# Performance work log

Hardware: AMD Instinct MI355X
Metric: run time of the kernel (lower is better)

## Reference

```python
import jax, jax.numpy as jnp
import numpy as np

B, N, D = 8, 10000, 16
E = 320000
EH, EOUT, NOUT = 32, 30, 64

def setup_inputs() -> dict:
    key = jax.random.key(0)
    ks = jax.random.split(key, 12)
    x = jax.random.normal(ks[0], (B, N, D), dtype=jnp.float32)
    edge_index = jax.random.randint(ks[1], (2, E), 0, N, dtype=jnp.int32)
    # edge_attr: col 0 = city distance (keep away from 0), col 1 = direction
    dist = jax.random.uniform(ks[2], (E,), dtype=jnp.float32) * 100.0 + 1.0
    direc = jax.random.uniform(ks[3], (E,), dtype=jnp.float32) * 360.0
    edge_attr = jnp.stack([dist, direc], axis=-1)
    wind_mean = jnp.array([3.0, 180.0], dtype=jnp.float32)
    wind_std = jnp.array([1.5, 90.0], dtype=jnp.float32)
    W1 = jax.random.normal(ks[4], (2 * D + 2 + 1, EH), dtype=jnp.float32) * 0.1
    b1 = jnp.zeros((EH,), dtype=jnp.float32)
    W2 = jax.random.normal(ks[5], (EH, EOUT), dtype=jnp.float32) * 0.1
    b2 = jnp.zeros((EOUT,), dtype=jnp.float32)
    Wn = jax.random.normal(ks[6], (EOUT, NOUT), dtype=jnp.float32) * 0.1
    bn = jnp.zeros((NOUT,), dtype=jnp.float32)
    return {"x": x, "edge_index": edge_index, "edge_attr": edge_attr,
            "wind_mean": wind_mean, "wind_std": wind_std,
            "W1": W1, "b1": b1, "W2": W2, "b2": b2, "Wn": Wn, "bn": bn}

def reference(x, edge_index, edge_attr, wind_mean, wind_std, W1, b1, W2, b2, Wn, bn):
    src, tgt = edge_index[0], edge_index[1]
    node_src = x[:, src]      # [B, E, D]
    node_tgt = x[:, tgt]      # [B, E, D]
    # de-normalize wind features (last 2 channels)
    src_wind = node_src[:, :, -2:] * wind_std[None, None, :] + wind_mean[None, None, :]
    speed = src_wind[:, :, 0]
    direc = src_wind[:, :, 1]
    city_dist = edge_attr[:, 0][None, :]   # [1, E]
    city_direc = edge_attr[:, 1][None, :]
    theta = jnp.abs(city_direc - direc)
    edge_weight = jax.nn.relu(3.0 * speed * jnp.cos(theta) / city_dist)  # [B, E]
    # normalized edge attributes (torch std is unbiased)
    ea_norm = (edge_attr - edge_attr.mean(axis=0)) / jnp.std(edge_attr, axis=0, ddof=1)
    ea_norm_b = jnp.broadcast_to(ea_norm[None, :, :], (x.shape[0], ea_norm.shape[0], 2))
    feat = jnp.concatenate([node_src, node_tgt, ea_norm_b, edge_weight[:, :, None]], axis=-1)  # [B, E, 2D+3]
    h = jax.nn.sigmoid(feat @ W1 + b1)
    e = jax.nn.sigmoid(h @ W2 + b2)        # [B, E, EOUT]
    agg = jnp.zeros((x.shape[0], x.shape[1], e.shape[-1]), dtype=e.dtype)
    agg = agg.at[:, tgt].add(e)
    agg = agg.at[:, src].add(-e)
    out = jax.nn.sigmoid(agg @ Wn + bn)    # [B, N, NOUT]
    return out
```

## Files before the change

kernel.cpp:

```cpp
#include <hip/hip_runtime.h>
#include <hip/hip_bf16.h>
#include <math.h>

#define B 8
#define N 10000
#define D 16
#define E 320000
#define EH 32
#define EOUT 30
#define NOUT 64
#define FEAT 35
#define FILL_BLOCKS ((E + 255) / 256)
#define PQ1K_BLOCKS ((B * N) / 16)

typedef short bf16x8 __attribute__((ext_vector_type(8)));
typedef float f32x4 __attribute__((ext_vector_type(4)));

#define LDS_FENCE() asm volatile("" ::: "memory")

__device__ __forceinline__ float sigmoidf_(float v) {
    return __builtin_amdgcn_rcpf(1.0f + __expf(-v));
}

__device__ __forceinline__ unsigned int pack_bf16_2(float a, float b) {
    unsigned ua = __float_as_uint(a), ub = __float_as_uint(b);
    ua = (ua + 0x7FFFu + ((ua >> 16) & 1u)) >> 16;
    ub = (ub + 0x7FFFu + ((ub >> 16) & 1u)) >> 16;
    return ua | (ub << 16);
}

__device__ __forceinline__ unsigned short bf16rn(float f) {
    unsigned u = __float_as_uint(f);
    u = (u + 0x7FFFu + ((u >> 16) & 1u)) >> 16;
    return (unsigned short)u;
}

__global__ void __launch_bounds__(256) stats_count_kernel(
    const float* __restrict__ ea, const int* __restrict__ eidx,
    float* __restrict__ stats, int* __restrict__ cnt)
{
    float s0 = 0.f, s1 = 0.f, q0 = 0.f, q1 = 0.f;
    for (int i = blockIdx.x * blockDim.x + threadIdx.x; i < E; i += gridDim.x * blockDim.x) {
        float2 v = *(const float2*)(ea + 2 * (size_t)i);
        s0 += v.x; q0 += v.x * v.x;
        s1 += v.y; q1 += v.y * v.y;
        atomicAdd(&cnt[eidx[E + i]], 1);
        atomicAdd(&cnt[N + eidx[i]], 1);
    }
    #pragma unroll
    for (int off = 32; off > 0; off >>= 1) {
        s0 += __shfl_down(s0, off);
        s1 += __shfl_down(s1, off);
        q0 += __shfl_down(q0, off);
        q1 += __shfl_down(q1, off);
    }
    if ((threadIdx.x & 63) == 0) {
        atomicAdd(&stats[0], s0);
        atomicAdd(&stats[1], s1);
        atomicAdd(&stats[2], q0);
        atomicAdd(&stats[3], q1);
    }
}

__global__ void __launch_bounds__(1024) scan_pq_kernel(
    const int* __restrict__ cnt_in, int* __restrict__ offs,
    int* __restrict__ cursor, float* __restrict__ stats,
    const float* __restrict__ W2, unsigned short* __restrict__ w2f,
    const float* __restrict__ x, const float* __restrict__ W1,
    const float* __restrict__ b1,
    unsigned short* __restrict__ Pb, unsigned short* __restrict__ Qb)
{
    if (blockIdx.x > 0) {
        int wid = (blockIdx.x - 1) * 16 + (threadIdx.x >> 6);
        int lane = threadIdx.x & 63;
        if (wid >= B * N) return;
        int j = lane & 31;
        int half = lane >> 5;
        const float* xr = x + (size_t)wid * D;
        float acc = half ? b1[j] : 0.f;
        const float* Wb = W1 + (half ? D * EH : 0);
        #pragma unroll
        for (int d = 0; d < D; d++)
            acc = fmaf(xr[d], Wb[d * EH + j], acc);
        float accN = __shfl_down(acc, 1);
        if (!(lane & 1)) {
            unsigned u = pack_bf16_2(acc, accN);
            unsigned short* dst = (half ? Qb : Pb) + (size_t)wid * EH + j;
            *(unsigned*)dst = u;
        }
        return;
    }

    if (threadIdx.x == 0) {
        const float n = (float)E;
        float s0 = stats[0], s1 = stats[1], q0 = stats[2], q1 = stats[3];
        float v0 = (q0 - s0 * s0 / n) / (n - 1.0f);
        float v1 = (q1 - s1 * s1 / n) / (n - 1.0f);
        stats[4] = s0 / n;
        stats[5] = 1.0f / sqrtf(v0);
        stats[6] = s1 / n;
        stats[7] = 1.0f / sqrtf(v1);
    }
    if (threadIdx.x < 128) {
        int tl = threadIdx.x >> 6;
        int ln = threadIdx.x & 63;
        int k0 = (ln >> 4) * 8;
        int col = tl * 16 + (ln & 15);
        unsigned short* hi = w2f + ((size_t)(tl * 2 + 0) * 64 + ln) * 8;
        unsigned short* lo = w2f + ((size_t)(tl * 2 + 1) * 64 + ln) * 8;
        #pragma unroll
        for (int j = 0; j < 8; j++) {
            float w = (col < EOUT) ? W2[(k0 + j) * EOUT + col] : 0.0f;
            unsigned u = __float_as_uint(w) & 0xFFFF0000u;
            float r = w - __uint_as_float(u);
            hi[j] = (unsigned short)(u >> 16);
            lo[j] = bf16rn(r);
        }
    }
    const int M = 2 * N;
    const int CH = 20;
    __shared__ int lds[1024];
    int t = threadIdx.x;
    int base = t * CH;
    int loc[CH];
    int s = 0;
    #pragma unroll
    for (int i = 0; i < CH; i++) {
        int idx = base + i;
        int v = (idx < M) ? cnt_in[idx] : 0;
        loc[i] = s;
        s += v;
    }
    lds[t] = s;
    __syncthreads();
    for (int off = 1; off < 1024; off <<= 1) {
        int v = (t >= off) ? lds[t - off] : 0;
        __syncthreads();
        lds[t] += v;
        __syncthreads();
    }
    int tbase = (t > 0) ? lds[t - 1] : 0;
    #pragma unroll
    for (int i = 0; i < CH; i++) {
        int idx = base + i;
        if (idx < M) {
            offs[idx] = tbase + loc[i];
            cursor[idx] = tbase + loc[i];
        }
    }
    if (t == 1023) offs[M] = lds[1023];
}

__global__ void __launch_bounds__(256) edge_mlp_kernel(
    const float* __restrict__ x, const int* __restrict__ eidx,
    const float* __restrict__ ea,
    const float* __restrict__ wind_mean, const float* __restrict__ wind_std,
    const float* __restrict__ W1, const float* __restrict__ b2,
    const float* __restrict__ stats,
    const unsigned short* __restrict__ Pb, const unsigned short* __restrict__ Qb,
    const unsigned short* __restrict__ w2f,
    unsigned short* __restrict__ eBuf,
    int* __restrict__ cursor, int* __restrict__ lists,
    int b0, int period, int ebOff)
{
    __shared__ unsigned short hsh[4][64][64];

    int bid = blockIdx.x;
    if (period) {
        int k = bid / period;
        int r = bid - k * period;
        if (r == period - 1) {
            int e = k * 256 + threadIdx.x;
            if (e < E) {
                int p = atomicAdd(&cursor[eidx[E + e]], 1);
                lists[p] = e;
                int q = atomicAdd(&cursor[N + eidx[e]], 1);
                lists[q] = e;
            }
            return;
        }
        bid -= k;
    }

    int t = bid * 256 + threadIdx.x;
    int bb = t / E;
    int e = t - bb * E;
    int b = b0 + bb;
    int wv = threadIdx.x >> 6;
    int lane = threadIdx.x & 63;

    int src = eidx[e];
    int tgt = eidx[E + e];

    const uint4* Pr = (const uint4*)(Pb + ((size_t)b * N + src) * EH);
    const uint4* Qr = (const uint4*)(Qb + ((size_t)b * N + tgt) * EH);

    float h[EH];
    #pragma unroll
    for (int i = 0; i < 4; i++) {
        uint4 p = Pr[i];
        uint4 q = Qr[i];
        unsigned pu[4] = {p.x, p.y, p.z, p.w};
        unsigned qu[4] = {q.x, q.y, q.z, q.w};
        #pragma unroll
        for (int k2 = 0; k2 < 4; k2++) {
            float pl = __uint_as_float(pu[k2] << 16);
            float ph = __uint_as_float(pu[k2] & 0xFFFF0000u);
            float ql = __uint_as_float(qu[k2] << 16);
            float qh = __uint_as_float(qu[k2] & 0xFFFF0000u);
            h[8 * i + 2 * k2 + 0] = pl + ql;
            h[8 * i + 2 * k2 + 1] = ph + qh;
        }
    }

    float2 eav = *(const float2*)(ea + 2 * (size_t)e);
    float dist = eav.x, cdir = eav.y;
    float f32v = (dist - stats[4]) * stats[5];
    float f33v = (cdir - stats[6]) * stats[7];

    float2 xw = *(const float2*)(x + ((size_t)b * N + src) * D + 14);
    float speed = xw.x * wind_std[0] + wind_mean[0];
    float sdir  = xw.y * wind_std[1] + wind_mean[1];
    float ew = fmaxf(3.0f * speed * __cosf(fabsf(cdir - sdir)) *
                     __builtin_amdgcn_rcpf(dist), 0.0f);

    const float* W1r32 = W1 + 32 * EH;
    const float* W1r33 = W1 + 33 * EH;
    const float* W1r34 = W1 + 34 * EH;
    #pragma unroll
    for (int j = 0; j < EH; j++) {
        float v = h[j];
        v = fmaf(f32v, W1r32[j], v);
        v = fmaf(f33v, W1r33[j], v);
        v = fmaf(ew,   W1r34[j], v);
        h[j] = sigmoidf_(v);
    }

    unsigned short* myrow = &hsh[wv][lane][0];
    int lx = lane & 7;
    #pragma unroll
    for (int i = 0; i < 4; i++) {
        unsigned hw[4];
        #pragma unroll
        for (int p = 0; p < 4; p++)
            hw[p] = pack_bf16_2(h[8 * i + 2 * p], h[8 * i + 2 * p + 1]);
        *(uint4*)(myrow + ((i ^ lx) << 3)) = make_uint4(hw[0], hw[1], hw[2], hw[3]);
    }
    LDS_FENCE();

    union { uint4 u; bf16x8 v; } bf[4];
    const uint4* wfp = (const uint4*)w2f;
    #pragma unroll
    for (int i = 0; i < 4; i++) bf[i].u = wfp[i * 64 + lane];

    int m  = lane & 15;
    int hr = lane >> 4;
    float bias0 = b2[m];
    float bias1 = (m < EOUT - 16) ? b2[16 + m] : 0.0f;

    f32x4 acc[4][2];
    #pragma unroll
    for (int g = 0; g < 4; g++) {
        f32x4 z0 = {bias0, bias0, bias0, bias0};
        f32x4 z1 = {bias1, bias1, bias1, bias1};
        acc[g][0] = z0;
        acc[g][1] = z1;
    }

    int mx = m & 7;
    #pragma unroll
    for (int g = 0; g < 4; g++) {
        const unsigned short* rp = &hsh[wv][g * 16 + m][0];
        bf16x8 Ah = *(const bf16x8*)(rp + ((hr ^ mx) << 3));
        acc[g][0] = __builtin_amdgcn_mfma_f32_16x16x32_bf16(Ah, bf[0].v, acc[g][0], 0, 0, 0);
        acc[g][1] = __builtin_amdgcn_mfma_f32_16x16x32_bf16(Ah, bf[2].v, acc[g][1], 0, 0, 0);
        acc[g][0] = __builtin_amdgcn_mfma_f32_16x16x32_bf16(Ah, bf[1].v, acc[g][0], 0, 0, 0);
        acc[g][1] = __builtin_amdgcn_mfma_f32_16x16x32_bf16(Ah, bf[3].v, acc[g][1], 0, 0, 0);
    }
    LDS_FENCE();

    unsigned short* wb = &hsh[wv][0][0];
    int c0 = m >> 3;
    int c1 = 2 + (m >> 3);
    int mp = m & 7;
    #pragma unroll
    for (int g = 0; g < 4; g++) {
        #pragma unroll
        for (int j = 0; j < 4; j++) {
            int er  = g * 16 + hr * 4 + j;
            int swz = ((hr & 1) << 2) | j;
            float v0 = sigmoidf_(acc[g][0][j]);
            float v1 = sigmoidf_(acc[g][1][j]);
            wb[er * 64 + ((c0 ^ swz) << 3) + mp] = bf16rn(v0);
            wb[er * 64 + ((c1 ^ swz) << 3) + mp] =
                (m < 14) ? bf16rn(v1) : (unsigned short)0;
        }
    }
    LDS_FENCE();

    int eWaveBase = e - lane;
    int rrow = lane >> 2;
    int rx   = rrow & 7;
    unsigned short* wdst = eBuf + ((size_t)(b - ebOff) * E + eWaveBase) * EH;
    #pragma unroll
    for (int i = 0; i < 4; i++) {
        uint4 v = *(const uint4*)(wb + (i * 16 + rrow) * 64 + (((lane & 3) ^ rx) << 3));
        *(uint4*)(wdst + i * 512 + lane * 8) = v;
    }
}

__global__ void __launch_bounds__(256) gather_kernel(
    const unsigned short* __restrict__ eBuf, const int* __restrict__ offs,
    const int* __restrict__ lists, const float* __restrict__ Wn,
    const float* __restrict__ bn, float* __restrict__ out,
    int b0, int nb, int ebOff)
{
    int wid = (blockIdx.x * blockDim.x + threadIdx.x) >> 6;
    int lane = threadIdx.x & 63;
    if (wid >= nb * N) return;
    int bb = wid / N;
    int node = wid - bb * N;
    int b = b0 + bb;

    int g = lane >> 2;
    int c = lane & 3;
    const uint4* ebase = (const uint4*)(eBuf + (size_t)(b - ebOff) * E * EH);

    float a0 = 0.f, a1 = 0.f, a2 = 0.f, a3 = 0.f;
    float a4 = 0.f, a5 = 0.f, a6 = 0.f, a7 = 0.f;

    {
        int s = offs[node], e1 = offs[node + 1];
        for (int r = s; r < e1; r += 16) {
            int row = r + g;
            if (row < e1) {
                int eid = lists[row];
                uint4 v = ebase[(size_t)eid * 4 + c];
                a0 += __uint_as_float(v.x << 16);
                a1 += __uint_as_float(v.x & 0xFFFF0000u);
                a2 += __uint_as_float(v.y << 16);
                a3 += __uint_as_float(v.y & 0xFFFF0000u);
                a4 += __uint_as_float(v.z << 16);
                a5 += __uint_as_float(v.z & 0xFFFF0000u);
                a6 += __uint_as_float(v.w << 16);
                a7 += __uint_as_float(v.w & 0xFFFF0000u);
            }
        }
    }
    {
        int s = offs[N + node], e1 = offs[N + node + 1];
        for (int r = s; r < e1; r += 16) {
            int row = r + g;
            if (row < e1) {
                int eid = lists[row];
                uint4 v = ebase[(size_t)eid * 4 + c];
                a0 -= __uint_as_float(v.x << 16);
                a1 -= __uint_as_float(v.x & 0xFFFF0000u);
                a2 -= __uint_as_float(v.y << 16);
                a3 -= __uint_as_float(v.y & 0xFFFF0000u);
                a4 -= __uint_as_float(v.z << 16);
                a5 -= __uint_as_float(v.z & 0xFFFF0000u);
                a6 -= __uint_as_float(v.w << 16);
                a7 -= __uint_as_float(v.w & 0xFFFF0000u);
            }
        }
    }

    #pragma unroll
    for (int off = 4; off <= 32; off <<= 1) {
        a0 += __shfl_xor(a0, off); a1 += __shfl_xor(a1, off);
        a2 += __shfl_xor(a2, off); a3 += __shfl_xor(a3, off);
        a4 += __shfl_xor(a4, off); a5 += __shfl_xor(a5, off);
        a6 += __shfl_xor(a6, off); a7 += __shfl_xor(a7, off);
    }

    float o = bn[lane];
    #pragma unroll
    for (int k = 0; k < EOUT; k++) {
        float av;
        switch (k & 7) {
            case 0:  av = a0; break;
            case 1:  av = a1; break;
            case 2:  av = a2; break;
            case 3:  av = a3; break;
            case 4:  av = a4; break;
            case 5:  av = a5; break;
            case 6:  av = a6; break;
            default: av = a7; break;
        }
        float ak = __shfl(av, k >> 3);
        o = fmaf(ak, Wn[k * NOUT + lane], o);
    }
    out[((size_t)b * N + node) * NOUT + lane] = sigmoidf_(o);
}

__global__ void __launch_bounds__(256) edge_kernel_atomic(
    const float* __restrict__ x, const int* __restrict__ eidx,
    const float* __restrict__ ea,
    const float* __restrict__ wind_mean, const float* __restrict__ wind_std,
    const float* __restrict__ W1, const float* __restrict__ b1,
    const float* __restrict__ W2, const float* __restrict__ b2,
    const float* __restrict__ stats, float* __restrict__ agg)
{
    int t = blockIdx.x * blockDim.x + threadIdx.x;
    if (t >= B * E) return;
    int b = t / E;
    int e = t - b * E;
    int src = eidx[e];
    int tgt = eidx[E + e];
    const float* xs = x + ((size_t)b * N + src) * D;
    const float* xt = x + ((size_t)b * N + tgt) * D;
    float f[FEAT];
    #pragma unroll
    for (int i = 0; i < D; i++) f[i] = xs[i];
    #pragma unroll
    for (int i = 0; i < D; i++) f[D + i] = xt[i];
    float2 eav = *(const float2*)(ea + 2 * (size_t)e);
    f[32] = (eav.x - stats[4]) * stats[5];
    f[33] = (eav.y - stats[6]) * stats[7];
    float speed = f[14] * wind_std[0] + wind_mean[0];
    float sdir  = f[15] * wind_std[1] + wind_mean[1];
    f[34] = fmaxf(3.0f * speed * cosf(fabsf(eav.y - sdir)) / eav.x, 0.0f);
    float h[EH];
    #pragma unroll
    for (int j = 0; j < EH; j++) h[j] = b1[j];
    #pragma unroll
    for (int k = 0; k < FEAT; k++) {
        float fk = f[k];
        #pragma unroll
        for (int j = 0; j < EH; j++) h[j] = fmaf(fk, W1[k * EH + j], h[j]);
    }
    #pragma unroll
    for (int j = 0; j < EH; j++) h[j] = sigmoidf_(h[j]);
    float o[EOUT];
    #pragma unroll
    for (int j = 0; j < EOUT; j++) o[j] = b2[j];
    #pragma unroll
    for (int k = 0; k < EH; k++) {
        float hk = h[k];
        #pragma unroll
        for (int j = 0; j < EOUT; j++) o[j] = fmaf(hk, W2[k * EOUT + j], o[j]);
    }
    float* at = agg + ((size_t)b * N + tgt) * EOUT;
    float* as = agg + ((size_t)b * N + src) * EOUT;
    #pragma unroll
    for (int j = 0; j < EOUT; j++) {
        float v = sigmoidf_(o[j]);
        atomicAdd(at + j,  v);
        atomicAdd(as + j, -v);
    }
}

__global__ void __launch_bounds__(256) node_kernel_fallback(
    const float* __restrict__ agg, const float* __restrict__ Wn,
    const float* __restrict__ bn, float* __restrict__ out)
{
    int t = blockIdx.x * blockDim.x + threadIdx.x;
    if (t >= B * N * NOUT) return;
    int row = t >> 6;
    int j   = t & 63;
    const float* a = agg + (size_t)row * EOUT;
    float acc = bn[j];
    #pragma unroll
    for (int k = 0; k < EOUT; k++) acc = fmaf(a[k], Wn[k * NOUT + j], acc);
    out[t] = sigmoidf_(acc);
}

extern "C" void kernel_launch(void* const* d_in, const int* in_sizes, int n_in,
                              void* d_out, int out_size, void* d_ws, size_t ws_size,
                              hipStream_t stream) {
    const float* x         = (const float*)d_in[0];
    const int*   eidx      = (const int*)d_in[1];
    const float* ea        = (const float*)d_in[2];
    const float* wind_mean = (const float*)d_in[3];
    const float* wind_std  = (const float*)d_in[4];
    const float* W1        = (const float*)d_in[5];
    const float* b1        = (const float*)d_in[6];
    const float* W2        = (const float*)d_in[7];
    const float* b2        = (const float*)d_in[8];
    const float* Wn        = (const float*)d_in[9];
    const float* bn        = (const float*)d_in[10];
    float* out = (float*)d_out;

    char* ws = (char*)d_ws;
    float*          stats = (float*)(ws + 0);
    unsigned short* w2f   = (unsigned short*)(ws + 256);
    int*            offs  = (int*)(ws + 4352);
    int*            cnt   = (int*)(ws + 84480);
    int*            lists = (int*)(ws + 164608);
    unsigned short* Pb    = (unsigned short*)(ws + 2724608);
    unsigned short* Qb    = (unsigned short*)(ws + 7844608);
    unsigned short* eBuf  = (unsigned short*)(ws + 12964608);
    const size_t fixed = 12964608;
    const size_t perBatch = (size_t)E * EH * sizeof(unsigned short);

    if (ws_size >= fixed + perBatch) {
        int chunk = (int)((ws_size - fixed) / perBatch);
        if (chunk > 8) chunk = 8;

        hipMemsetAsync(ws, 0, 164608, stream);

        stats_count_kernel<<<256, 256, 0, stream>>>(ea, eidx, stats, cnt);
        scan_pq_kernel<<<1 + PQ1K_BLOCKS, 1024, 0, stream>>>(
            cnt, offs, cnt, stats, W2, w2f, x, W1, b1, Pb, Qb);

        for (int b0 = 0; b0 < B; b0 += chunk) {
            int nb = B - b0; if (nb > chunk) nb = chunk;
            int eblk = nb * E / 256;
            int period = (b0 == 0) ? (nb + 1) : 0;
            int grid = eblk + ((b0 == 0) ? FILL_BLOCKS : 0);
            edge_mlp_kernel<<<grid, 256, 0, stream>>>(
                x, eidx, ea, wind_mean, wind_std, W1, b2, stats,
                Pb, Qb, w2f, eBuf, cnt, lists, b0, period, b0);
            gather_kernel<<<nb * (N * 64 / 256), 256, 0, stream>>>(
                eBuf, offs, lists, Wn, bn, out, b0, nb, b0);
        }
    } else {
        float* agg = (float*)(ws + 164608);
        size_t zero_bytes = 164608 + (size_t)B * N * EOUT * sizeof(float);
        hipMemsetAsync(ws, 0, zero_bytes, stream);
        stats_count_kernel<<<256, 256, 0, stream>>>(ea, eidx, stats, cnt);
        scan_pq_kernel<<<1, 1024, 0, stream>>>(
            cnt, offs, cnt, stats, W2, w2f, x, W1, b1,
            (unsigned short*)(ws + 256), (unsigned short*)(ws + 256));
        int nwork = B * E;
        edge_kernel_atomic<<<(nwork + 255) / 256, 256, 0, stream>>>(
            x, eidx, ea, wind_mean, wind_std, W1, b1, W2, b2, stats, agg);
        int nout_elems = B * N * NOUT;
        node_kernel_fallback<<<(nout_elems + 255) / 256, 256, 0, stream>>>(
            agg, Wn, bn, out);
    }
}
```

Before: 355.2 us.

## Scatter edge outputs into CSR-sorted positions so gather reads contiguously

The fill stage now runs as its own kernel and records each edge's slot in the incoming and outgoing CSR lists. The edge MLP kernel writes each edge's result twice, directly at those slots, so the gather kernel reads rows sequentially with no lists indirection. This removes the random gathers and index loads from the gather, in exchange for doubling the edge buffer writes, making those writes scattered, and adding a separate launch. Because the per-batch footprint doubles, fewer batches fit per chunk.

New measurement: 404.0 us. 1.14x slower.

```diff
diff --git a/kernel.cpp b/kernel.cpp
--- a/kernel.cpp
+++ b/kernel.cpp
@@ -151,6 +151,18 @@
     if (t == 1023) offs[M] = lds[1023];
 }
 
+__global__ void __launch_bounds__(256) fill_kernel(
+    const int* __restrict__ eidx, int* __restrict__ cursor,
+    int* __restrict__ pos)
+{
+    int e = blockIdx.x * 256 + threadIdx.x;
+    if (e >= E) return;
+    int p = atomicAdd(&cursor[eidx[E + e]], 1);
+    pos[e] = p;
+    int q = atomicAdd(&cursor[N + eidx[e]], 1);
+    pos[E + e] = q;
+}
+
 __global__ void __launch_bounds__(256) edge_mlp_kernel(
     const float* __restrict__ x, const int* __restrict__ eidx,
     const float* __restrict__ ea,
@@ -159,30 +171,13 @@
     const float* __restrict__ stats,
     const unsigned short* __restrict__ Pb, const unsigned short* __restrict__ Qb,
     const unsigned short* __restrict__ w2f,
-    unsigned short* __restrict__ eBuf,
-    int* __restrict__ cursor, int* __restrict__ lists,
-    int b0, int period, int ebOff)
+    unsigned short* __restrict__ eBuf2,
+    const int* __restrict__ pos,
+    int b0, int ebOff)
 {
     __shared__ unsigned short hsh[4][64][64];
 
-    int bid = blockIdx.x;
-    if (period) {
-        int k = bid / period;
-        int r = bid - k * period;
-        if (r == period - 1) {
-            int e = k * 256 + threadIdx.x;
-            if (e < E) {
-                int p = atomicAdd(&cursor[eidx[E + e]], 1);
-                lists[p] = e;
-                int q = atomicAdd(&cursor[N + eidx[e]], 1);
-                lists[q] = e;
-            }
-            return;
-        }
-        bid -= k;
-    }
-
-    int t = bid * 256 + threadIdx.x;
+    int t = blockIdx.x * 256 + threadIdx.x;
     int bb = t / E;
     int e = t - bb * E;
     int b = b0 + bb;
@@ -301,17 +296,22 @@
     int eWaveBase = e - lane;
     int rrow = lane >> 2;
     int rx   = rrow & 7;
-    unsigned short* wdst = eBuf + ((size_t)(b - ebOff) * E + eWaveBase) * EH;
+    unsigned short* eb2 = eBuf2 + (size_t)(b - ebOff) * (2 * E) * EH;
     #pragma unroll
     for (int i = 0; i < 4; i++) {
-        uint4 v = *(const uint4*)(wb + (i * 16 + rrow) * 64 + (((lane & 3) ^ rx) << 3));
-        *(uint4*)(wdst + i * 512 + lane * 8) = v;
+        int row = i * 16 + rrow;
+        uint4 v = *(const uint4*)(wb + row * 64 + (((lane & 3) ^ rx) << 3));
+        int eg   = eWaveBase + row;
+        int pin  = pos[eg];
+        int pout = pos[E + eg];
+        *(uint4*)(eb2 + (size_t)pin  * EH + (lane & 3) * 8) = v;
+        *(uint4*)(eb2 + (size_t)pout * EH + (lane & 3) * 8) = v;
     }
 }
 
 __global__ void __launch_bounds__(256) gather_kernel(
-    const unsigned short* __restrict__ eBuf, const int* __restrict__ offs,
-    const int* __restrict__ lists, const float* __restrict__ Wn,
+    const unsigned short* __restrict__ eBuf2, const int* __restrict__ offs,
+    const float* __restrict__ Wn,
     const float* __restrict__ bn, float* __restrict__ out,
     int b0, int nb, int ebOff)
 {
@@ -324,7 +324,7 @@
 
     int g = lane >> 2;
     int c = lane & 3;
-    const uint4* ebase = (const uint4*)(eBuf + (size_t)(b - ebOff) * E * EH);
+    const uint4* ebase = (const uint4*)(eBuf2 + (size_t)(b - ebOff) * (2 * E) * EH);
 
     float a0 = 0.f, a1 = 0.f, a2 = 0.f, a3 = 0.f;
     float a4 = 0.f, a5 = 0.f, a6 = 0.f, a7 = 0.f;
@@ -334,8 +334,7 @@
         for (int r = s; r < e1; r += 16) {
             int row = r + g;
             if (row < e1) {
-                int eid = lists[row];
-                uint4 v = ebase[(size_t)eid * 4 + c];
+                uint4 v = ebase[(size_t)row * 4 + c];
                 a0 += __uint_as_float(v.x << 16);
                 a1 += __uint_as_float(v.x & 0xFFFF0000u);
                 a2 += __uint_as_float(v.y << 16);
@@ -352,8 +351,7 @@
         for (int r = s; r < e1; r += 16) {
             int row = r + g;
             if (row < e1) {
-                int eid = lists[row];
-                uint4 v = ebase[(size_t)eid * 4 + c];
+                uint4 v = ebase[(size_t)row * 4 + c];
                 a0 -= __uint_as_float(v.x << 16);
                 a1 -= __uint_as_float(v.x & 0xFFFF0000u);
                 a2 -= __uint_as_float(v.y << 16);
@@ -487,15 +485,15 @@
     unsigned short* w2f   = (unsigned short*)(ws + 256);
     int*            offs  = (int*)(ws + 4352);
     int*            cnt   = (int*)(ws + 84480);
-    int*            lists = (int*)(ws + 164608);
+    int*            pos   = (int*)(ws + 164608);
     unsigned short* Pb    = (unsigned short*)(ws + 2724608);
     unsigned short* Qb    = (unsigned short*)(ws + 7844608);
-    unsigned short* eBuf  = (unsigned short*)(ws + 12964608);
+    unsigned short* eBuf2 = (unsigned short*)(ws + 12964608);
     const size_t fixed = 12964608;
-    const size_t perBatch = (size_t)E * EH * sizeof(unsigned short);
-
-    if (ws_size >= fixed + perBatch) {
-        int chunk = (int)((ws_size - fixed) / perBatch);
+    const size_t perBatch2 = (size_t)(2 * E) * EH * sizeof(unsigned short);
+
+    if (ws_size >= fixed + perBatch2) {
+        int chunk = (int)((ws_size - fixed) / perBatch2);
         if (chunk > 8) chunk = 8;
 
         hipMemsetAsync(ws, 0, 164608, stream);
@@ -503,17 +501,15 @@
         stats_count_kernel<<<256, 256, 0, stream>>>(ea, eidx, stats, cnt);
         scan_pq_kernel<<<1 + PQ1K_BLOCKS, 1024, 0, stream>>>(
             cnt, offs, cnt, stats, W2, w2f, x, W1, b1, Pb, Qb);
+        fill_kernel<<<FILL_BLOCKS, 256, 0, stream>>>(eidx, cnt, pos);
 
         for (int b0 = 0; b0 < B; b0 += chunk) {
             int nb = B - b0; if (nb > chunk) nb = chunk;
-            int eblk = nb * E / 256;
-            int period = (b0 == 0) ? (nb + 1) : 0;
-            int grid = eblk + ((b0 == 0) ? FILL_BLOCKS : 0);
-            edge_mlp_kernel<<<grid, 256, 0, stream>>>(
+            edge_mlp_kernel<<<nb * (E / 256), 256, 0, stream>>>(
                 x, eidx, ea, wind_mean, wind_std, W1, b2, stats,
-                Pb, Qb, w2f, eBuf, cnt, lists, b0, period, b0);
+                Pb, Qb, w2f, eBuf2, pos, b0, b0);
             gather_kernel<<<nb * (N * 64 / 256), 256, 0, stream>>>(
-                eBuf, offs, lists, Wn, bn, out, b0, nb, b0);
+                eBuf2, offs, Wn, bn, out, b0, nb, b0);
         }
     } else {
         float* agg = (float*)(ws + 164608);
```
